# Kernel optimization log

Measured on AMD Instinct MI355X. Metric: run time of the kernel, lower is better.

## Reference

```python
import jax, jax.numpy as jnp
import numpy as np

B, S = 32, 256          # sequences, tokens per sequence (prefill)
DIM, NH, NKV, HD = 2048, 16, 16, 128
CLS, GRID, BASE = 1, 16, 10000


def precompute_freqs_cis_2d(grid_size, n_elem, base, cls_token_num):
    half = n_elem // 2
    freqs = 1.0 / (base ** (np.arange(0, half, 2)[: half // 2].astype(np.float32) / half))
    t = np.arange(grid_size, dtype=np.float32)
    fr = np.outer(t, freqs)                      # [grid, half//2]
    fg = np.concatenate([
        np.broadcast_to(fr[:, None, :], (grid_size, grid_size, fr.shape[1])),
        np.broadcast_to(fr[None, :, :], (grid_size, grid_size, fr.shape[1])),
    ], axis=-1)                                  # [grid, grid, half]
    cache = np.stack([np.cos(fg), np.sin(fg)], axis=-1).reshape(grid_size * grid_size, half, 2)
    cond = np.concatenate([np.zeros((cls_token_num, half, 2), np.float32), cache.astype(np.float32)], axis=0)
    return jnp.asarray(cond)                     # [cls+grid^2, half, 2]

FREQS = precompute_freqs_cis_2d(GRID, HD, BASE, CLS)


def _apply_rope(x, fc):
    # x: [T, H, HD], fc: [T, HD//2, 2]
    xr = x.reshape(x.shape[0], x.shape[1], HD // 2, 2)
    c = fc[:, None, :, 0]
    s = fc[:, None, :, 1]
    out = jnp.stack([xr[..., 0] * c - xr[..., 1] * s,
                     xr[..., 1] * c + xr[..., 0] * s], axis=-1)
    return out.reshape(x.shape)


def setup_inputs() -> dict:
    key = jax.random.key(0)
    k1, k2, k3 = jax.random.split(key, 3)
    x = jax.random.normal(k1, (B * S, DIM), dtype=jnp.float32)
    positions = jnp.tile(jnp.arange(S, dtype=jnp.int32), B)  # per-seq positions 0..S-1
    total_kv = (NH + 2 * NKV) * HD
    wqkv = jax.random.normal(k2, (total_kv, DIM), dtype=jnp.float32) * 0.02
    wo = jax.random.normal(k3, (DIM, DIM), dtype=jnp.float32) * 0.02
    return {"x": x, "positions": positions, "wqkv": wqkv, "wo": wo}


def reference(x, positions, wqkv, wo):
    T = x.shape[0]
    kv_size = NKV * HD
    qkv = x @ wqkv.T                               # [T, dim + 2*kv_size]
    xq, xk, xv = jnp.split(qkv, [DIM, DIM + kv_size], axis=-1)
    q = xq.reshape(T, NH, HD)
    k = xk.reshape(T, NKV, HD)
    v = xv.reshape(T, NKV, HD)

    fc = FREQS[positions]                          # [T, HD//2, 2]
    q = _apply_rope(q, fc)
    k = _apply_rope(k, fc)

    # paged attention (prefill): causal attention within each sequence
    qb = q.reshape(B, S, NH, HD)
    kb = k.reshape(B, S, NKV, HD)
    vb = v.reshape(B, S, NKV, HD)
    scale = HD ** -0.5
    scores = jnp.einsum("bqhd,bkhd->bhqk", qb, kb) * scale   # [B,H,S,S]
    causal = jnp.tril(jnp.ones((S, S), dtype=bool))
    scores = jnp.where(causal[None, None], scores, jnp.finfo(scores.dtype).min)
    attn = jax.nn.softmax(scores, axis=-1)
    out = jnp.einsum("bhqk,bkhd->bqhd", attn, vb).reshape(T, DIM)
    return out @ wo.T
```

## Files before the change

kernel.cpp:

```cpp
#include <hip/hip_runtime.h>
#include <cstddef>


typedef float    f32x4 __attribute__((ext_vector_type(4)));
typedef _Float16 f16x8 __attribute__((ext_vector_type(8)));
typedef _Float16 f16x4 __attribute__((ext_vector_type(4)));

#define LOG2E 1.4426950408889634f

__device__ static inline f32x4 mfma16x32(f16x8 a, f16x8 b, f32x4 c) {
  return __builtin_amdgcn_mfma_f32_16x16x32_f16(a, b, c, 0, 0, 0);
}

__device__ static inline void gload16(const void* g, void* lds) {
  __builtin_amdgcn_global_load_lds(
      (const __attribute__((address_space(1))) unsigned int*)g,
      (__attribute__((address_space(3))) unsigned int*)lds, 16, 0, 0);
}

#define BAR()    asm volatile("s_barrier" ::: "memory")
#define VMCNT6() asm volatile("s_waitcnt vmcnt(6)" ::: "memory")

__global__ void cvt_f32_f16(const float* __restrict__ src,
                            _Float16* __restrict__ dst, int n4) {
  int i = blockIdx.x * blockDim.x + threadIdx.x;
  if (i >= n4) return;
  f32x4 v = *(const f32x4*)(src + (size_t)i * 4);
  f16x4 o;
  o[0] = (_Float16)v[0]; o[1] = (_Float16)v[1];
  o[2] = (_Float16)v[2]; o[3] = (_Float16)v[3];
  *(f16x4*)(dst + (size_t)i * 4) = o;
}

template <typename OutT>
__global__ void __launch_bounds__(512, 2)
gemm_bt3(const _Float16* __restrict__ A, const _Float16* __restrict__ Bt,
         OutT* __restrict__ C, int M, int N, int K) {
  __shared__ __attribute__((aligned(16))) _Float16 Ab[2][256 * 64];
  __shared__ __attribute__((aligned(16))) _Float16 Bb[2][256 * 64];

  const int tid  = threadIdx.x;
  const int lane = tid & 63;
  const int w    = tid >> 6;
  const int wm   = w >> 2, wn = w & 3;
  const int g    = lane >> 4, li = lane & 15;

  const int nwg = (int)gridDim.x;
  const int cpx = nwg >> 3;
  const int bid = (int)blockIdx.x;
  const int swz = (bid & 7) * cpx + (bid >> 3);
  const int nbn = N >> 8;
  const int bm  = (swz / nbn) << 8;
  const int bn  = (swz % nbn) << 8;
  const int NT  = K >> 6;

  const int srow = tid >> 3;
  const int scol = ((tid & 7) ^ (srow & 7)) * 8;
  const _Float16* gA = A  + (size_t)(bm + srow) * K + scol;
  const _Float16* gB = Bt + (size_t)(bn + srow) * K + scol;
  const int sdst = w * 1024;

  auto stage = [&](const _Float16* gbase, _Float16* lbase, int h, int kt) {
    const _Float16* gp = gbase + (size_t)h * 128 * K + kt;
    char* lp = (char*)lbase + h * 16384;
#pragma unroll
    for (int j = 0; j < 2; ++j)
      gload16(gp + (size_t)j * 64 * K, lp + j * 8192 + sdst);
  };

  auto rdfrag = [&](const _Float16* buf, int row, int k2) -> f16x8 {
    const int pc = ((k2 << 2) + g) ^ (li & 7);
    return *(const f16x8*)((const char*)buf + row * 128 + pc * 16);
  };

  f32x4 acc[8][4] = {};

  stage(gA, Ab[0], 0, 0);
  stage(gB, Bb[0], 0, 0);
  stage(gB, Bb[0], 1, 0);
  stage(gA, Ab[0], 1, 0);
  stage(gA, Ab[1], 0, (NT > 1) ? 64 : 0);
  VMCNT6();
  BAR();

  for (int T = 0; T < NT; ++T) {
    const int cb = T & 1, nb = cb ^ 1;
    const _Float16* Ac = Ab[cb];
    const _Float16* Bc = Bb[cb];
    const int ktN  = (T + 1 < NT) ? (T + 1) << 6 : 0;
    const int ktN2 = (T + 2 < NT) ? (T + 2) << 6 : 0;

    f16x8 af0[4][2], af1[4][2], bf0[2][2], bf1[2][2];

#pragma unroll
    for (int m = 0; m < 4; ++m)
#pragma unroll
      for (int k2 = 0; k2 < 2; ++k2)
        af0[m][k2] = rdfrag(Ac, wm * 128 + m * 16 + li, k2);
#pragma unroll
    for (int n = 0; n < 2; ++n)
#pragma unroll
      for (int k2 = 0; k2 < 2; ++k2)
        bf0[n][k2] = rdfrag(Bc, wn * 64 + n * 16 + li, k2);
    stage(gB, Bb[nb], 0, ktN);
    BAR();
    __builtin_amdgcn_s_setprio(1);
#pragma unroll
    for (int m = 0; m < 4; ++m)
#pragma unroll
      for (int n = 0; n < 2; ++n)
#pragma unroll
        for (int k2 = 0; k2 < 2; ++k2)
          acc[m][n] = mfma16x32(af0[m][k2], bf0[n][k2], acc[m][n]);
    __builtin_amdgcn_s_setprio(0);
    VMCNT6();
    BAR();

#pragma unroll
    for (int n = 0; n < 2; ++n)
#pragma unroll
      for (int k2 = 0; k2 < 2; ++k2)
        bf1[n][k2] = rdfrag(Bc, wn * 64 + (n + 2) * 16 + li, k2);
    stage(gB, Bb[nb], 1, ktN);
    BAR();
    __builtin_amdgcn_s_setprio(1);
#pragma unroll
    for (int m = 0; m < 4; ++m)
#pragma unroll
      for (int n = 0; n < 2; ++n)
#pragma unroll
        for (int k2 = 0; k2 < 2; ++k2)
          acc[m][n + 2] = mfma16x32(af0[m][k2], bf1[n][k2], acc[m][n + 2]);
    __builtin_amdgcn_s_setprio(0);
    VMCNT6();
    BAR();

#pragma unroll
    for (int m = 0; m < 4; ++m)
#pragma unroll
      for (int k2 = 0; k2 < 2; ++k2)
        af1[m][k2] = rdfrag(Ac, wm * 128 + (m + 4) * 16 + li, k2);
    stage(gA, Ab[nb], 1, ktN);
    BAR();
    __builtin_amdgcn_s_setprio(1);
#pragma unroll
    for (int m = 0; m < 4; ++m)
#pragma unroll
      for (int n = 0; n < 2; ++n)
#pragma unroll
        for (int k2 = 0; k2 < 2; ++k2)
          acc[m + 4][n] = mfma16x32(af1[m][k2], bf0[n][k2], acc[m + 4][n]);
    __builtin_amdgcn_s_setprio(0);
    VMCNT6();
    BAR();

    stage(gA, Ab[cb], 0, ktN2);
    BAR();
    __builtin_amdgcn_s_setprio(1);
#pragma unroll
    for (int m = 0; m < 4; ++m)
#pragma unroll
      for (int n = 0; n < 2; ++n)
#pragma unroll
        for (int k2 = 0; k2 < 2; ++k2)
          acc[m + 4][n + 2] = mfma16x32(af1[m][k2], bf1[n][k2], acc[m + 4][n + 2]);
    __builtin_amdgcn_s_setprio(0);
    VMCNT6();
    BAR();
  }

  asm volatile("s_waitcnt vmcnt(0)" ::: "memory");

#pragma unroll
  for (int m = 0; m < 8; ++m)
#pragma unroll
    for (int n = 0; n < 4; ++n)
#pragma unroll
      for (int r = 0; r < 4; ++r) {
        const int row = bm + wm * 128 + m * 16 + g * 4 + r;
        const int col = bn + wn * 64 + n * 16 + li;
        C[(size_t)row * N + col] = (OutT)acc[m][n][r];
      }
}

__global__ void rope_kernel(_Float16* __restrict__ qkv,
                            const int* __restrict__ positions) {
  const int idx = blockIdx.x * blockDim.x + threadIdx.x;
  const int ch = idx & 15;
  const int hh = (idx >> 4) & 31;
  const int t  = idx >> 9;
  _Float16* p = qkv + (size_t)t * 6144 + hh * 128 + ch * 8;
  const int pos = positions[t];
  f16x8 v = *(const f16x8*)p;
  f16x8 o;
  if (pos == 0) {
#pragma unroll
    for (int u = 0; u < 8; ++u) o[u] = (_Float16)0.f;
  } else {
    const int gi = pos - 1;
    const float tv = (ch < 8) ? (float)(gi >> 4) : (float)(gi & 15);
#pragma unroll
    for (int u = 0; u < 4; ++u) {
      const int k2 = (ch * 4 + u) & 31;
      const float freq = exp2f((float)k2 * (-13.287712379549449f / 32.0f));
      const float ang = tv * freq;
      float s, c;
      sincosf(ang, &s, &c);
      const float x0 = (float)v[2 * u];
      const float x1 = (float)v[2 * u + 1];
      o[2 * u]     = (_Float16)(x0 * c - x1 * s);
      o[2 * u + 1] = (_Float16)(x1 * c + x0 * s);
    }
  }
  *(f16x8*)p = o;
}

__global__ void __launch_bounds__(512)
attn_kernel(const _Float16* __restrict__ qkv, _Float16* __restrict__ O) {
  const int b  = blockIdx.x >> 4;
  const int h  = blockIdx.x & 15;
  const int tb = b << 8;
  const int tid = threadIdx.x;
  const int lane = tid & 63;
  const int w = tid >> 6;
  const int g = lane >> 4, li = lane & 15;

  __shared__ __attribute__((aligned(16))) _Float16 Ks[64 * 128];
  __shared__ __attribute__((aligned(16))) _Float16 Vt[128 * 64];
  __shared__ __attribute__((aligned(16))) _Float16 Ps[8][32 * 40];

  f16x8 qf[2][4];
#pragma unroll
  for (int rb = 0; rb < 2; ++rb)
#pragma unroll
    for (int ks = 0; ks < 4; ++ks)
      qf[rb][ks] = *(const f16x8*)(qkv + (size_t)(tb + w * 32 + rb * 16 + li) * 6144
                                   + h * 128 + ks * 32 + g * 8);

  f32x4 oacc[2][8] = {};
  float m_r[2][4], l_r[2][4];
#pragma unroll
  for (int rb = 0; rb < 2; ++rb)
#pragma unroll
    for (int r = 0; r < 4; ++r) { m_r[rb][r] = -1e30f; l_r[rb][r] = 0.f; }

  const float scale = 0.08838834764831845f;

  for (int kt = 0; kt < 4; ++kt) {
#pragma unroll
    for (int i = 0; i < 2; ++i) {
      const int s = i * 512 + tid;
      const int key = s >> 4;
      const int sch = (s & 15) ^ (key & 7);
      const _Float16* gk = qkv + (size_t)(tb + kt * 64 + key) * 6144
                           + 2048 + h * 128 + sch * 8;
      gload16(gk, (char*)Ks + (i * 512 + (tid & ~63)) * 16);
    }
#pragma unroll
    for (int i = 0; i < 2; ++i) {
      const int s = i * 512 + tid;
      const int key = s >> 4;
      const int chv = s & 15;
      f16x8 v = *(const f16x8*)(qkv + (size_t)(tb + kt * 64 + key) * 6144
                                + 4096 + h * 128 + chv * 8);
#pragma unroll
      for (int e = 0; e < 8; ++e) {
        const int d = chv * 8 + e;
        const int blk = ((key >> 3) ^ (d & 7) ^ ((d >> 3) & 7)) & 7;
        Vt[d * 64 + blk * 8 + (key & 7)] = v[e];
      }
    }
    __syncthreads();

    if (kt <= (w >> 1)) {
      f32x4 sacc[2][4] = {};
#pragma unroll
      for (int ks = 0; ks < 4; ++ks) {
        f16x8 kf[4];
#pragma unroll
        for (int cb = 0; cb < 4; ++cb) {
          const int key = cb * 16 + li;
          const int chunk = (ks * 4 + g) ^ (key & 7);
          kf[cb] = *(const f16x8*)((const char*)Ks + key * 256 + chunk * 16);
        }
#pragma unroll
        for (int rb = 0; rb < 2; ++rb)
#pragma unroll
          for (int cb = 0; cb < 4; ++cb)
            sacc[rb][cb] = mfma16x32(qf[rb][ks], kf[cb], sacc[rb][cb]);
      }
#pragma unroll
      for (int rb = 0; rb < 2; ++rb) {
#pragma unroll
        for (int r = 0; r < 4; ++r) {
          const int q = w * 32 + rb * 16 + g * 4 + r;
          float mx = -1e30f;
#pragma unroll
          for (int cb = 0; cb < 4; ++cb) {
            float sv = sacc[rb][cb][r] * scale;
            const int key = kt * 64 + cb * 16 + li;
            sv = (key <= q) ? sv : -1e30f;
            sacc[rb][cb][r] = sv;
            mx = fmaxf(mx, sv);
          }
#pragma unroll
          for (int off = 1; off < 16; off <<= 1)
            mx = fmaxf(mx, __shfl_xor(mx, off));
          const float mold = m_r[rb][r];
          const float mnew = fmaxf(mold, mx);
          const float alpha = exp2f((mold - mnew) * LOG2E);
          float rsum = 0.f;
#pragma unroll
          for (int cb = 0; cb < 4; ++cb) {
            const float pv = exp2f((sacc[rb][cb][r] - mnew) * LOG2E);
            sacc[rb][cb][r] = pv;
            rsum += pv;
          }
#pragma unroll
          for (int off = 1; off < 16; off <<= 1)
            rsum += __shfl_xor(rsum, off);
          m_r[rb][r] = mnew;
          l_r[rb][r] = l_r[rb][r] * alpha + rsum;
#pragma unroll
          for (int db = 0; db < 8; ++db)
            oacc[rb][db][r] *= alpha;
        }
      }
#pragma unroll
      for (int ks2 = 0; ks2 < 2; ++ks2) {
#pragma unroll
        for (int rb = 0; rb < 2; ++rb)
#pragma unroll
          for (int cbh = 0; cbh < 2; ++cbh) {
            const int cb = ks2 * 2 + cbh;
#pragma unroll
            for (int r = 0; r < 4; ++r)
              Ps[w][(rb * 16 + g * 4 + r) * 40 + cbh * 16 + li] =
                  (_Float16)sacc[rb][cb][r];
          }
        asm volatile("s_waitcnt lgkmcnt(0)" ::: "memory");
        f16x8 pa[2];
#pragma unroll
        for (int rb = 0; rb < 2; ++rb)
          pa[rb] = *(const f16x8*)(&Ps[w][(rb * 16 + li) * 40 + g * 8]);
#pragma unroll
        for (int db = 0; db < 8; ++db) {
          const int d = db * 16 + li;
          const int keych = ks2 * 4 + g;
          const int blk = (keych ^ (d & 7) ^ ((d >> 3) & 7)) & 7;
          const f16x8 vf = *(const f16x8*)(&Vt[d * 64 + blk * 8]);
#pragma unroll
          for (int rb = 0; rb < 2; ++rb)
            oacc[rb][db] = mfma16x32(pa[rb], vf, oacc[rb][db]);
        }
      }
    }
    __syncthreads();
  }
#pragma unroll
  for (int rb = 0; rb < 2; ++rb)
#pragma unroll
    for (int db = 0; db < 8; ++db)
#pragma unroll
      for (int r = 0; r < 4; ++r) {
        const int row = tb + w * 32 + rb * 16 + g * 4 + r;
        const int col = h * 128 + db * 16 + li;
        O[(size_t)row * 2048 + col] = (_Float16)(oacc[rb][db][r] / l_r[rb][r]);
      }
}

extern "C" void kernel_launch(void* const* d_in, const int* in_sizes, int n_in,
                              void* d_out, int out_size, void* d_ws, size_t ws_size,
                              hipStream_t stream) {
  const float* x         = (const float*)d_in[0];
  const int*   positions = (const int*)d_in[1];
  const float* wqkv      = (const float*)d_in[2];
  const float* wo        = (const float*)d_in[3];
  float* out = (float*)d_out;

  char* ws = (char*)d_ws;
  _Float16* qkv    = (_Float16*)(ws);
  _Float16* xf     = (_Float16*)(ws + 100663296);
  _Float16* wqkvf  = (_Float16*)(ws + 134217728);
  _Float16* wof    = (_Float16*)(ws + 159383552);
  _Float16* of     = xf;

  cvt_f32_f16<<<16384, 256, 0, stream>>>(x, xf, 4194304);
  cvt_f32_f16<<<12288, 256, 0, stream>>>(wqkv, wqkvf, 3145728);
  cvt_f32_f16<<< 4096, 256, 0, stream>>>(wo, wof, 1048576);

  gemm_bt3<_Float16><<<768, 512, 0, stream>>>(xf, wqkvf, qkv, 8192, 6144, 2048);

  rope_kernel<<<16384, 256, 0, stream>>>(qkv, positions);

  attn_kernel<<<512, 512, 0, stream>>>(qkv, of);

  gemm_bt3<float><<<256, 512, 0, stream>>>(of, wof, out, 8192, 2048, 2048);
}
```

Before: 382.1 us.

## Merge conversions, deepen GEMM prefetch, and balance causal attention across waves

```diff
diff --git a/kernel.cpp b/kernel.cpp
--- a/kernel.cpp
+++ b/kernel.cpp
@@ -7,6 +7,7 @@
 typedef _Float16 f16x4 __attribute__((ext_vector_type(4)));
 
 #define LOG2E 1.4426950408889634f
+#define NLOG2B_32 (-0.41524101186192697f)
 
 __device__ static inline f32x4 mfma16x32(f16x8 a, f16x8 b, f32x4 c) {
   return __builtin_amdgcn_mfma_f32_16x16x32_f16(a, b, c, 0, 0, 0);
@@ -19,12 +20,16 @@
 }
 
 #define BAR()    asm volatile("s_barrier" ::: "memory")
-#define VMCNT6() asm volatile("s_waitcnt vmcnt(6)" ::: "memory")
-
-__global__ void cvt_f32_f16(const float* __restrict__ src,
-                            _Float16* __restrict__ dst, int n4) {
+#define VMCNT8() asm volatile("s_waitcnt vmcnt(8)" ::: "memory")
+
+__global__ void cvt3_f32_f16(const float* __restrict__ s0, _Float16* __restrict__ d0,
+                             const float* __restrict__ s1, _Float16* __restrict__ d1,
+                             const float* __restrict__ s2, _Float16* __restrict__ d2) {
   int i = blockIdx.x * blockDim.x + threadIdx.x;
-  if (i >= n4) return;
+  const float* src; _Float16* dst;
+  if (i < 4194304)      { src = s0; dst = d0; }
+  else if (i < 7340032) { src = s1; dst = d1; i -= 4194304; }
+  else                  { src = s2; dst = d2; i -= 7340032; }
   f32x4 v = *(const f32x4*)(src + (size_t)i * 4);
   f16x4 o;
   o[0] = (_Float16)v[0]; o[1] = (_Float16)v[1];
@@ -34,7 +39,7 @@
 
 template <typename OutT>
 __global__ void __launch_bounds__(512, 2)
-gemm_bt3(const _Float16* __restrict__ A, const _Float16* __restrict__ Bt,
+gemm_bt4(const _Float16* __restrict__ A, const _Float16* __restrict__ Bt,
          OutT* __restrict__ C, int M, int N, int K) {
   __shared__ __attribute__((aligned(16))) _Float16 Ab[2][256 * 64];
   __shared__ __attribute__((aligned(16))) _Float16 Bb[2][256 * 64];
@@ -75,19 +80,18 @@
 
   f32x4 acc[8][4] = {};
 
-  stage(gA, Ab[0], 0, 0);
-  stage(gB, Bb[0], 0, 0);
-  stage(gB, Bb[0], 1, 0);
-  stage(gA, Ab[0], 1, 0);
-  stage(gA, Ab[1], 0, (NT > 1) ? 64 : 0);
-  VMCNT6();
+  stage(gA, Ab[0], 0, 0); stage(gB, Bb[0], 0, 0);
+  stage(gB, Bb[0], 1, 0); stage(gA, Ab[0], 1, 0);
+  const int k1 = (NT > 1) ? 64 : 0;
+  stage(gA, Ab[1], 0, k1); stage(gB, Bb[1], 0, k1);
+  stage(gB, Bb[1], 1, k1); stage(gA, Ab[1], 1, k1);
+  VMCNT8();
   BAR();
 
   for (int T = 0; T < NT; ++T) {
-    const int cb = T & 1, nb = cb ^ 1;
+    const int cb = T & 1;
     const _Float16* Ac = Ab[cb];
     const _Float16* Bc = Bb[cb];
-    const int ktN  = (T + 1 < NT) ? (T + 1) << 6 : 0;
     const int ktN2 = (T + 2 < NT) ? (T + 2) << 6 : 0;
 
     f16x8 af0[4][2], af1[4][2], bf0[2][2], bf1[2][2];
@@ -102,7 +106,6 @@
 #pragma unroll
       for (int k2 = 0; k2 < 2; ++k2)
         bf0[n][k2] = rdfrag(Bc, wn * 64 + n * 16 + li, k2);
-    stage(gB, Bb[nb], 0, ktN);
     BAR();
     __builtin_amdgcn_s_setprio(1);
 #pragma unroll
@@ -113,7 +116,6 @@
         for (int k2 = 0; k2 < 2; ++k2)
           acc[m][n] = mfma16x32(af0[m][k2], bf0[n][k2], acc[m][n]);
     __builtin_amdgcn_s_setprio(0);
-    VMCNT6();
     BAR();
 
 #pragma unroll
@@ -121,7 +123,6 @@
 #pragma unroll
       for (int k2 = 0; k2 < 2; ++k2)
         bf1[n][k2] = rdfrag(Bc, wn * 64 + (n + 2) * 16 + li, k2);
-    stage(gB, Bb[nb], 1, ktN);
     BAR();
     __builtin_amdgcn_s_setprio(1);
 #pragma unroll
@@ -132,7 +133,6 @@
         for (int k2 = 0; k2 < 2; ++k2)
           acc[m][n + 2] = mfma16x32(af0[m][k2], bf1[n][k2], acc[m][n + 2]);
     __builtin_amdgcn_s_setprio(0);
-    VMCNT6();
     BAR();
 
 #pragma unroll
@@ -140,7 +140,8 @@
 #pragma unroll
       for (int k2 = 0; k2 < 2; ++k2)
         af1[m][k2] = rdfrag(Ac, wm * 128 + (m + 4) * 16 + li, k2);
-    stage(gA, Ab[nb], 1, ktN);
+    stage(gB, Bb[cb], 0, ktN2);
+    stage(gB, Bb[cb], 1, ktN2);
     BAR();
     __builtin_amdgcn_s_setprio(1);
 #pragma unroll
@@ -151,10 +152,10 @@
         for (int k2 = 0; k2 < 2; ++k2)
           acc[m + 4][n] = mfma16x32(af1[m][k2], bf0[n][k2], acc[m + 4][n]);
     __builtin_amdgcn_s_setprio(0);
-    VMCNT6();
     BAR();
 
     stage(gA, Ab[cb], 0, ktN2);
+    stage(gA, Ab[cb], 1, ktN2);
     BAR();
     __builtin_amdgcn_s_setprio(1);
 #pragma unroll
@@ -165,7 +166,7 @@
         for (int k2 = 0; k2 < 2; ++k2)
           acc[m + 4][n + 2] = mfma16x32(af1[m][k2], bf1[n][k2], acc[m + 4][n + 2]);
     __builtin_amdgcn_s_setprio(0);
-    VMCNT6();
+    VMCNT8();
     BAR();
   }
 
@@ -202,7 +203,7 @@
 #pragma unroll
     for (int u = 0; u < 4; ++u) {
       const int k2 = (ch * 4 + u) & 31;
-      const float freq = exp2f((float)k2 * (-13.287712379549449f / 32.0f));
+      const float freq = exp2f((float)k2 * NLOG2B_32);
       const float ang = tv * freq;
       float s, c;
       sincosf(ang, &s, &c);
@@ -229,12 +230,16 @@
   __shared__ __attribute__((aligned(16))) _Float16 Vt[128 * 64];
   __shared__ __attribute__((aligned(16))) _Float16 Ps[8][32 * 40];
 
+  const int qb[2]   = {w, 15 - w};
+  const int qrow[2] = {qb[0] * 16, qb[1] * 16};
+  const int kmax[2] = {qb[0] >> 2, qb[1] >> 2};
+
   f16x8 qf[2][4];
 #pragma unroll
   for (int rb = 0; rb < 2; ++rb)
 #pragma unroll
     for (int ks = 0; ks < 4; ++ks)
-      qf[rb][ks] = *(const f16x8*)(qkv + (size_t)(tb + w * 32 + rb * 16 + li) * 6144
+      qf[rb][ks] = *(const f16x8*)(qkv + (size_t)(tb + qrow[rb] + li) * 6144
                                    + h * 128 + ks * 32 + g * 8);
 
   f32x4 oacc[2][8] = {};
@@ -272,7 +277,8 @@
     }
     __syncthreads();
 
-    if (kt <= (w >> 1)) {
+    const bool act[2] = {kt <= kmax[0], kt <= kmax[1]};
+    if (act[0] || act[1]) {
       f32x4 sacc[2][4] = {};
 #pragma unroll
       for (int ks = 0; ks < 4; ++ks) {
@@ -285,15 +291,17 @@
         }
 #pragma unroll
         for (int rb = 0; rb < 2; ++rb)
-#pragma unroll
-          for (int cb = 0; cb < 4; ++cb)
-            sacc[rb][cb] = mfma16x32(qf[rb][ks], kf[cb], sacc[rb][cb]);
+          if (act[rb])
+#pragma unroll
+            for (int cb = 0; cb < 4; ++cb)
+              sacc[rb][cb] = mfma16x32(qf[rb][ks], kf[cb], sacc[rb][cb]);
       }
 #pragma unroll
       for (int rb = 0; rb < 2; ++rb) {
+        if (!act[rb]) continue;
 #pragma unroll
         for (int r = 0; r < 4; ++r) {
-          const int q = w * 32 + rb * 16 + g * 4 + r;
+          const int q = qrow[rb] + g * 4 + r;
           float mx = -1e30f;
 #pragma unroll
           for (int cb = 0; cb < 4; ++cb) {
@@ -329,7 +337,8 @@
 #pragma unroll
       for (int ks2 = 0; ks2 < 2; ++ks2) {
 #pragma unroll
-        for (int rb = 0; rb < 2; ++rb)
+        for (int rb = 0; rb < 2; ++rb) {
+          if (!act[rb]) continue;
 #pragma unroll
           for (int cbh = 0; cbh < 2; ++cbh) {
             const int cb = ks2 * 2 + cbh;
@@ -338,11 +347,13 @@
               Ps[w][(rb * 16 + g * 4 + r) * 40 + cbh * 16 + li] =
                   (_Float16)sacc[rb][cb][r];
           }
+        }
         asm volatile("s_waitcnt lgkmcnt(0)" ::: "memory");
         f16x8 pa[2];
 #pragma unroll
         for (int rb = 0; rb < 2; ++rb)
-          pa[rb] = *(const f16x8*)(&Ps[w][(rb * 16 + li) * 40 + g * 8]);
+          if (act[rb])
+            pa[rb] = *(const f16x8*)(&Ps[w][(rb * 16 + li) * 40 + g * 8]);
 #pragma unroll
         for (int db = 0; db < 8; ++db) {
           const int d = db * 16 + li;
@@ -351,7 +362,8 @@
           const f16x8 vf = *(const f16x8*)(&Vt[d * 64 + blk * 8]);
 #pragma unroll
           for (int rb = 0; rb < 2; ++rb)
-            oacc[rb][db] = mfma16x32(pa[rb], vf, oacc[rb][db]);
+            if (act[rb])
+              oacc[rb][db] = mfma16x32(pa[rb], vf, oacc[rb][db]);
         }
       }
     }
@@ -363,7 +375,7 @@
     for (int db = 0; db < 8; ++db)
 #pragma unroll
       for (int r = 0; r < 4; ++r) {
-        const int row = tb + w * 32 + rb * 16 + g * 4 + r;
+        const int row = tb + qrow[rb] + g * 4 + r;
         const int col = h * 128 + db * 16 + li;
         O[(size_t)row * 2048 + col] = (_Float16)(oacc[rb][db][r] / l_r[rb][r]);
       }
@@ -385,15 +397,13 @@
   _Float16* wof    = (_Float16*)(ws + 159383552);
   _Float16* of     = xf;
 
-  cvt_f32_f16<<<16384, 256, 0, stream>>>(x, xf, 4194304);
-  cvt_f32_f16<<<12288, 256, 0, stream>>>(wqkv, wqkvf, 3145728);
-  cvt_f32_f16<<< 4096, 256, 0, stream>>>(wo, wof, 1048576);
-
-  gemm_bt3<_Float16><<<768, 512, 0, stream>>>(xf, wqkvf, qkv, 8192, 6144, 2048);
+  cvt3_f32_f16<<<32768, 256, 0, stream>>>(x, xf, wqkv, wqkvf, wo, wof);
+
+  gemm_bt4<_Float16><<<768, 512, 0, stream>>>(xf, wqkvf, qkv, 8192, 6144, 2048);
 
   rope_kernel<<<16384, 256, 0, stream>>>(qkv, positions);
 
   attn_kernel<<<512, 512, 0, stream>>>(qkv, of);
 
-  gemm_bt3<float><<<256, 512, 0, stream>>>(of, wof, out, 8192, 2048, 2048);
-}
+  gemm_bt4<float><<<256, 512, 0, stream>>>(of, wof, out, 8192, 2048, 2048);
+}
```

After: 427.3 us. +11.8%, slower.
